# Optimization experiments

Measured on AMD Instinct MI355X. Metric: run time of the kernel, lower is better.

## Reference

```python
import jax, jax.numpy as jnp
import numpy as np

WS = 8
NUM_HEADS = 8
EMBED_DIM = 256
LN_EPS = 1e-5


def setup_inputs() -> dict:
    key = jax.random.key(0)
    ks = jax.random.split(key, 5)
    b, c, h, w = 4, EMBED_DIM, 128, 128
    return {
        "x": jax.random.normal(ks[0], (b, c, h, w), dtype=jnp.float32),
        "in_proj_w": jax.random.normal(ks[1], (3 * c, c), dtype=jnp.float32) * 0.02,
        "in_proj_b": jax.random.normal(ks[2], (3 * c,), dtype=jnp.float32) * 0.02,
        "out_w": jax.random.normal(ks[3], (c, c), dtype=jnp.float32) * 0.02,
        "out_b": jax.random.normal(ks[4], (c,), dtype=jnp.float32) * 0.02,
        "ln_w": jnp.ones((c,), dtype=jnp.float32),
        "ln_b": jnp.zeros((c,), dtype=jnp.float32),
    }


def reference(x, in_proj_w, in_proj_b, out_w, out_b, ln_w, ln_b):
    b, c, h, w = x.shape
    pad_h = (-h) % WS
    pad_w = (-w) % WS
    xp = jnp.pad(x, ((0, 0), (0, 0), (0, pad_h), (0, pad_w)))
    Hp, Wp = h + pad_h, w + pad_w
    h1, w1 = Hp // WS, Wp // WS
    L = h1 * w1            # attention sequence = number of windows
    N = b * WS * WS        # attention batch = b * within-window positions
    # rearrange 'b c (h1 h2) (w1 w2) -> (h1 w1) (b h2 w2) c', then batch-first
    t = xp.reshape(b, c, h1, WS, w1, WS)
    t = jnp.transpose(t, (2, 4, 0, 3, 5, 1)).reshape(L, N, c)
    t = jnp.transpose(t, (1, 0, 2))  # [N, L, c]
    # nn.MultiheadAttention (self-attention, no mask)
    qkv = t @ in_proj_w.T + in_proj_b  # [N, L, 3c]
    q, k, v = jnp.split(qkv, 3, axis=-1)
    D = c // NUM_HEADS
    q = q.reshape(N, L, NUM_HEADS, D) * (D ** -0.5)
    k = k.reshape(N, L, NUM_HEADS, D)
    v = v.reshape(N, L, NUM_HEADS, D)
    attn = jax.nn.softmax(jnp.einsum('nlhd,nmhd->nhlm', q, k), axis=-1)
    o = jnp.einsum('nhlm,nmhd->nlhd', attn, v).reshape(N, L, c)
    o = o @ out_w.T + out_b
    # LayerNorm over channel dim
    mu = jnp.mean(o, axis=-1, keepdims=True)
    var = jnp.mean(jnp.square(o - mu), axis=-1, keepdims=True)
    o = (o - mu) * jax.lax.rsqrt(var + LN_EPS) * ln_w + ln_b
    # inverse rearrange '(h1 w1) (b h2 w2) c -> b c (h1 h2) (w1 w2)'
    y = jnp.transpose(o, (1, 0, 2)).reshape(h1, w1, b, WS, WS, c)
    y = jnp.transpose(y, (2, 5, 0, 3, 1, 4)).reshape(b, c, Hp, Wp)
    return y[:, :, :h, :w]
```

## Files before the change

### kernel.cpp

```cpp
#include <hip/hip_runtime.h>
#include <stdint.h>
#include <stddef.h>


typedef __attribute__((ext_vector_type(8))) short bf16x8;
typedef __attribute__((ext_vector_type(4))) float f32x4;
typedef __attribute__((ext_vector_type(16))) float f32x16;
typedef __attribute__((ext_vector_type(4))) unsigned u32x4;
typedef __attribute__((ext_vector_type(2))) unsigned u32x2;
typedef unsigned short bf16u;

#define LOG2E 1.4426950408889634f
#define MFMA32(a, b, c) __builtin_amdgcn_mfma_f32_32x32x16_bf16(a, b, c, 0, 0, 0)

__device__ __forceinline__ bf16u f2b(float f) {
  uint32_t u = __float_as_uint(f);
  u += 0x7fffu + ((u >> 16) & 1u);
  return (bf16u)(u >> 16);
}
__device__ __forceinline__ float b2f(bf16u s) {
  return __uint_as_float(((uint32_t)s) << 16);
}

__device__ __forceinline__ void gload_lds16(const void* g, void* l) {
  __builtin_amdgcn_global_load_lds((__attribute__((address_space(1))) void*)(g),
                                   (__attribute__((address_space(3))) void*)(l),
                                   16, 0, 0);
}

__device__ __forceinline__ unsigned cvtpk(float a, float b) {
  unsigned r;
  asm("v_cvt_pk_bf16_f32 %0, %1, %2" : "=v"(r) : "v"(a), "v"(b));
  return r;
}

__device__ __forceinline__ float frcp(float x) {
  float r;
  asm("v_rcp_f32 %0, %1" : "=v"(r) : "v"(x));
  return r;
}

__device__ __forceinline__ void swap32(unsigned a, unsigned b, bool hi,
                                       unsigned& x, unsigned& y) {
#if __has_builtin(__builtin_amdgcn_permlane32_swap)
  typedef __attribute__((ext_vector_type(2))) unsigned uint2v;
  uint2v r = __builtin_amdgcn_permlane32_swap(a, b, false, false);
  x = r.x;
  y = r.y;
#else
  unsigned as = (unsigned)__shfl_xor((int)a, 32);
  unsigned bs = (unsigned)__shfl_xor((int)b, 32);
  x = hi ? bs : a;
  y = hi ? b : as;
#endif
}

__global__ __launch_bounds__(256) void k_convert2(const float* __restrict__ s1,
                                                  const float* __restrict__ s2,
                                                  bf16u* __restrict__ d1,
                                                  bf16u* __restrict__ d2) {
  int i = blockIdx.x * 256 + threadIdx.x;
  if (i < 768 * 256) d1[i] = f2b(s1[i]);
  else { int j = i - 768 * 256; d2[j] = f2b(s2[j]); }
}

__global__ __launch_bounds__(256) void k_rearrange(const float* __restrict__ x,
                                                   bf16u* __restrict__ Tb) {
  const int bid = blockIdx.x;
  const int ct = bid & 7, hh = (bid >> 3) & 127, b = bid >> 10;
  const int c0 = ct * 32;
  const int h1 = hh >> 3, h2 = hh & 7;
  __shared__ float tile[32][129];
  for (int e = threadIdx.x; e < 4096; e += 256) {
    int cc = e >> 7, ww = e & 127;
    tile[cc][ww] = x[(((size_t)(b * 256 + c0 + cc)) * 128 + hh) * 128 + ww];
  }
  __syncthreads();
  for (int e = threadIdx.x; e < 4096; e += 256) {
    int ww = e >> 5, cc = e & 31;
    int w1 = ww >> 3, w2 = ww & 7;
    int i = ((b * 64 + h2 * 8 + w2) << 8) | (h1 * 16 + w1);
    Tb[(size_t)i * 256 + c0 + cc] = f2b(tile[cc][ww]);
  }
}

__global__ __launch_bounds__(256) void k_qkv(const bf16u* __restrict__ Tb,
                                             const bf16u* __restrict__ Wb,
                                             const float* __restrict__ bias,
                                             bf16u* __restrict__ Qb,
                                             bf16u* __restrict__ Kb,
                                             bf16u* __restrict__ Vtb) {
  __shared__ bf16u As[128 * 64];
  __shared__ bf16u Bs[128 * 64];
  const int bid0 = blockIdx.x;
  const int bid = (bid0 & 7) * 384 + (bid0 >> 3);
  const int o0 = (bid % 6) * 128;
  const int i0 = (bid / 6) * 128;
  const int seg = o0 >> 8;
  const int t = threadIdx.x;
  const int lane = t & 63, lo = lane & 15, hi = lane >> 4;
  const int w = t >> 6, wr = w >> 1, wc = w & 1;
  const int rr = t >> 3, cc8 = t & 7;
  f32x4 acc[4][4] = {};
  for (int k0 = 0; k0 < 256; k0 += 64) {
    __syncthreads();
#pragma unroll
    for (int j = 0; j < 4; ++j) {
      const int row = j * 32 + rr;
      const int sc = (cc8 ^ (row & 7)) * 8;
      bf16u* const da = As + (j * 32 + w * 8) * 64;
      bf16u* const db = Bs + (j * 32 + w * 8) * 64;
      gload_lds16(Tb + (size_t)(i0 + row) * 256 + k0 + sc, da);
      gload_lds16(Wb + (size_t)(o0 + row) * 256 + k0 + sc, db);
    }
    __syncthreads();
#pragma unroll
    for (int ks = 0; ks < 2; ++ks) {
      bf16x8 af[4], bf_[4];
#pragma unroll
      for (int m = 0; m < 4; ++m) {
        const int row = wr * 64 + m * 16 + lo;
        const int c = (ks * 4 + hi) ^ (lo & 7);
        af[m] = *(const bf16x8*)&As[row * 64 + c * 8];
      }
#pragma unroll
      for (int nn = 0; nn < 4; ++nn) {
        const int row = wc * 64 + nn * 16 + lo;
        const int c = (ks * 4 + hi) ^ (lo & 7);
        bf_[nn] = *(const bf16x8*)&Bs[row * 64 + c * 8];
      }
#pragma unroll
      for (int m = 0; m < 4; ++m)
#pragma unroll
        for (int nn = 0; nn < 4; ++nn)
          acc[m][nn] = __builtin_amdgcn_mfma_f32_16x16x32_bf16(af[m], bf_[nn], acc[m][nn], 0, 0, 0);
    }
  }
  const float oscale = (seg == 0) ? (0.17677669529663687f * LOG2E) : 1.0f;
#pragma unroll
  for (int m = 0; m < 4; ++m) {
#pragma unroll
    for (int nn = 0; nn < 4; ++nn) {
      const int o = o0 + wc * 64 + nn * 16 + lo;
      const int within = o & 255, head = within >> 5, dd = within & 31;
      const float bia = bias[o];
      const int tok0 = i0 + wr * 64 + m * 16 + hi * 4;
      const int nt = tok0 >> 8, ls0 = tok0 & 255;
      if (seg == 2) {
        float v0 = acc[m][nn][0] + bia, v1 = acc[m][nn][1] + bia;
        float v2 = acc[m][nn][2] + bia, v3 = acc[m][nn][3] + bia;
        u32x2 pkd = {cvtpk(v0, v1), cvtpk(v2, v3)};
        *(u32x2*)(Vtb + ((size_t)((nt * 8 + head) * 32 + dd)) * 256 + ls0) = pkd;
      } else {
        bf16u* const dst = (seg == 0) ? Qb : Kb;
#pragma unroll
        for (int r = 0; r < 4; ++r) {
          float v = (acc[m][nn][r] + bia) * oscale;
          dst[((size_t)((nt * 8 + head) * 256 + ls0 + r)) * 32 + dd] = f2b(v);
        }
      }
    }
  }
}

__global__ __launch_bounds__(256, 2) void k_attn(const bf16u* __restrict__ Qb,
                                                 const bf16u* __restrict__ Kb,
                                                 const bf16u* __restrict__ Vtb,
                                                 bf16u* __restrict__ Ob) {
  const int nh = blockIdx.x;
  const int n = nh >> 3, h = nh & 7;
  const bf16u* Qp = Qb + (size_t)nh * 8192;
  const bf16u* Kp = Kb + (size_t)nh * 8192;
  const bf16u* Vp = Vtb + (size_t)nh * 8192;
  const int t = threadIdx.x, w = t >> 6, lane = t & 63;
  const int l31 = lane & 31;
  const bool hi5 = (lane & 32) != 0;

  bf16x8 qf[2][2];
#pragma unroll
  for (int qs = 0; qs < 2; ++qs)
#pragma unroll
    for (int dh = 0; dh < 2; ++dh)
      qf[qs][dh] = *(const bf16x8*)(Qp + (size_t)(w * 64 + qs * 32 + l31) * 32 +
                                    dh * 16 + (hi5 ? 8 : 0));

  const bf16u* kbase = Kp + (size_t)l31 * 32 + (hi5 ? 8 : 0);
  const bf16u* vbase = Vp + (size_t)l31 * 256 + (hi5 ? 8 : 0);

  bf16x8 kf0 = *(const bf16x8*)(kbase);
  bf16x8 kf1 = *(const bf16x8*)(kbase + 16);
  bf16x8 vf0 = *(const bf16x8*)(vbase);
  bf16x8 vf1 = *(const bf16x8*)(vbase + 16);

  const u32x4 onesu = {0x3f803f80u, 0x3f803f80u, 0x3f803f80u, 0x3f803f80u};
  const bf16x8 onesf = __builtin_bit_cast(bf16x8, onesu);

  f32x16 accO[2] = {};
  f32x16 accS[2] = {};

#pragma unroll
  for (int kt = 0; kt < 8; ++kt) {
    const int nkt = (kt + 1) & 7;
    bf16x8 nk0 = *(const bf16x8*)(kbase + nkt * 1024);
    bf16x8 nk1 = *(const bf16x8*)(kbase + nkt * 1024 + 16);
    bf16x8 nv0 = *(const bf16x8*)(vbase + nkt * 32);
    bf16x8 nv1 = *(const bf16x8*)(vbase + nkt * 32 + 16);

#pragma unroll
    for (int qs = 0; qs < 2; ++qs) {
      f32x16 s = {};
      s = MFMA32(kf0, qf[qs][0], s);
      s = MFMA32(kf1, qf[qs][1], s);
      unsigned pk[8];
#pragma unroll
      for (int jp = 0; jp < 8; ++jp)
        pk[jp] = cvtpk(exp2f(s[2 * jp]), exp2f(s[2 * jp + 1]));
      unsigned x0, x1, x2, x3, y0, y1, y2, y3;
      swap32(pk[0], pk[2], hi5, x0, x2);
      swap32(pk[1], pk[3], hi5, x1, x3);
      swap32(pk[4], pk[6], hi5, y0, y2);
      swap32(pk[5], pk[7], hi5, y1, y3);
      u32x4 pa0 = {x0, x1, x2, x3};
      u32x4 pa1 = {y0, y1, y2, y3};
      const bf16x8 a0 = __builtin_bit_cast(bf16x8, pa0);
      const bf16x8 a1 = __builtin_bit_cast(bf16x8, pa1);
      __builtin_amdgcn_s_setprio(1);
      accO[qs] = MFMA32(a0, vf0, accO[qs]);
      accO[qs] = MFMA32(a1, vf1, accO[qs]);
      accS[qs] = MFMA32(a0, onesf, accS[qs]);
      accS[qs] = MFMA32(a1, onesf, accS[qs]);
      __builtin_amdgcn_s_setprio(0);
    }
    kf0 = nk0;
    kf1 = nk1;
    vf0 = nv0;
    vf1 = nv1;
  }
#pragma unroll
  for (int qs = 0; qs < 2; ++qs) {
#pragma unroll
    for (int r = 0; r < 16; ++r) {
      int row = (r & 3) + 8 * (r >> 2) + ((lane & 32) >> 3);
      float o = accO[qs][r] * frcp(accS[qs][r]);
      Ob[((size_t)(n * 256 + w * 64 + qs * 32 + row)) * 256 + h * 32 + l31] = f2b(o);
    }
  }
}

__global__ __launch_bounds__(256) void k_out(const bf16u* __restrict__ Ob,
                                             const bf16u* __restrict__ Wb,
                                             const float* __restrict__ bias,
                                             const float* __restrict__ lnw,
                                             const float* __restrict__ lnb,
                                             bf16u* __restrict__ On) {
  __shared__ bf16u As[64 * 64];
  __shared__ bf16u Bs[256 * 64];
  __shared__ float red[64][4][2];
  const int i0 = blockIdx.x * 64;
  const int t = threadIdx.x, w = t >> 6, lane = t & 63, lo = lane & 15, hi = lane >> 4;
  const int rr = t >> 3, cc8 = t & 7;
  f32x4 acc[4][4] = {};
  for (int k0 = 0; k0 < 256; k0 += 64) {
    __syncthreads();
#pragma unroll
    for (int j = 0; j < 2; ++j) {
      const int row = j * 32 + rr;
      const int sc = (cc8 ^ (row & 7)) * 8;
      gload_lds16(Ob + (size_t)(i0 + row) * 256 + k0 + sc,
                  As + (j * 32 + w * 8) * 64);
    }
#pragma unroll
    for (int j = 0; j < 8; ++j) {
      const int row = j * 32 + rr;
      const int sc = (cc8 ^ (row & 7)) * 8;
      gload_lds16(Wb + (size_t)row * 256 + k0 + sc,
                  Bs + (j * 32 + w * 8) * 64);
    }
    __syncthreads();
#pragma unroll
    for (int ks = 0; ks < 2; ++ks) {
      bf16x8 af[4], bf_[4];
#pragma unroll
      for (int m = 0; m < 4; ++m) {
        const int row = m * 16 + lo;
        const int c = (ks * 4 + hi) ^ (lo & 7);
        af[m] = *(const bf16x8*)&As[row * 64 + c * 8];
      }
#pragma unroll
      for (int nn = 0; nn < 4; ++nn) {
        const int row = w * 64 + nn * 16 + lo;
        const int c = (ks * 4 + hi) ^ (lo & 7);
        bf_[nn] = *(const bf16x8*)&Bs[row * 64 + c * 8];
      }
#pragma unroll
      for (int m = 0; m < 4; ++m)
#pragma unroll
        for (int nn = 0; nn < 4; ++nn)
          acc[m][nn] = __builtin_amdgcn_mfma_f32_16x16x32_bf16(af[m], bf_[nn], acc[m][nn], 0, 0, 0);
    }
  }
#pragma unroll
  for (int m = 0; m < 4; ++m)
#pragma unroll
    for (int nn = 0; nn < 4; ++nn) {
      float bia = bias[w * 64 + nn * 16 + lo];
#pragma unroll
      for (int r = 0; r < 4; ++r) acc[m][nn][r] += bia;
    }
#pragma unroll
  for (int m = 0; m < 4; ++m)
#pragma unroll
    for (int r = 0; r < 4; ++r) {
      float sv = acc[m][0][r] + acc[m][1][r] + acc[m][2][r] + acc[m][3][r];
      float sq = acc[m][0][r] * acc[m][0][r] + acc[m][1][r] * acc[m][1][r] +
                 acc[m][2][r] * acc[m][2][r] + acc[m][3][r] * acc[m][3][r];
      sv += __shfl_xor(sv, 1); sq += __shfl_xor(sq, 1);
      sv += __shfl_xor(sv, 2); sq += __shfl_xor(sq, 2);
      sv += __shfl_xor(sv, 4); sq += __shfl_xor(sq, 4);
      sv += __shfl_xor(sv, 8); sq += __shfl_xor(sq, 8);
      if (lo == 0) {
        red[m * 16 + hi * 4 + r][w][0] = sv;
        red[m * 16 + hi * 4 + r][w][1] = sq;
      }
    }
  __syncthreads();
#pragma unroll
  for (int m = 0; m < 4; ++m)
#pragma unroll
    for (int r = 0; r < 4; ++r) {
      int row = m * 16 + hi * 4 + r;
      float S  = red[row][0][0] + red[row][1][0] + red[row][2][0] + red[row][3][0];
      float Q2 = red[row][0][1] + red[row][1][1] + red[row][2][1] + red[row][3][1];
      float mu = S * 0.00390625f;
      float var = Q2 * 0.00390625f - mu * mu;
      float rstd = rsqrtf(var + 1e-5f);
#pragma unroll
      for (int nn = 0; nn < 4; ++nn) {
        int oc = w * 64 + nn * 16 + lo;
        float o = (acc[m][nn][r] - mu) * rstd * lnw[oc] + lnb[oc];
        On[(size_t)(i0 + row) * 256 + oc] = f2b(o);
      }
    }
}

__global__ __launch_bounds__(256) void k_unrearrange(const bf16u* __restrict__ On,
                                                     float* __restrict__ y) {
  const int bid = blockIdx.x;
  const int ct = bid & 7, hh = (bid >> 3) & 127, b = bid >> 10;
  const int c0 = ct * 32;
  const int h1 = hh >> 3, h2 = hh & 7;
  __shared__ float tile[32][129];
  for (int e = threadIdx.x; e < 4096; e += 256) {
    int ww = e >> 5, cc = e & 31;
    int w1 = ww >> 3, w2 = ww & 7;
    int i = ((b * 64 + h2 * 8 + w2) << 8) | (h1 * 16 + w1);
    tile[cc][ww] = b2f(On[(size_t)i * 256 + c0 + cc]);
  }
  __syncthreads();
  for (int e = threadIdx.x; e < 4096; e += 256) {
    int cc = e >> 7, ww = e & 127;
    y[(((size_t)(b * 256 + c0 + cc)) * 128 + hh) * 128 + ww] = tile[cc][ww];
  }
}

extern "C" void kernel_launch(void* const* d_in, const int* in_sizes, int n_in,
                              void* d_out, int out_size, void* d_ws, size_t ws_size,
                              hipStream_t stream) {
  const float* x     = (const float*)d_in[0];
  const float* w_qkv = (const float*)d_in[1];
  const float* b_qkv = (const float*)d_in[2];
  const float* w_out = (const float*)d_in[3];
  const float* b_out = (const float*)d_in[4];
  const float* ln_w  = (const float*)d_in[5];
  const float* ln_b  = (const float*)d_in[6];
  float* y = (float*)d_out;

  const size_t SEG = 33554432;
  char* ws = (char*)d_ws;
  if (ws_size < 5 * SEG + 768 * 256 * 2 + 256 * 256 * 2) return;
  bf16u* Tb = (bf16u*)(ws);
  bf16u* Qb = (bf16u*)(ws + SEG);
  bf16u* Kb = (bf16u*)(ws + 2 * SEG);
  bf16u* Vtb = (bf16u*)(ws + 3 * SEG);
  bf16u* Ob = (bf16u*)(ws + 4 * SEG);
  bf16u* Wqkvb = (bf16u*)(ws + 5 * SEG);
  bf16u* Woutb = (bf16u*)(ws + 5 * SEG + 768 * 256 * 2);
  bf16u* On = Tb;

  k_convert2<<<1024, 256, 0, stream>>>(w_qkv, w_out, Wqkvb, Woutb);
  k_rearrange<<<4096, 256, 0, stream>>>(x, Tb);
  k_qkv<<<3072, 256, 0, stream>>>(Tb, Wqkvb, b_qkv, Qb, Kb, Vtb);
  k_attn<<<2048, 256, 0, stream>>>(Qb, Kb, Vtb, Ob);
  k_out<<<1024, 256, 0, stream>>>(Ob, Woutb, b_out, ln_w, ln_b, On);
  k_unrearrange<<<4096, 256, 0, stream>>>(On, y);
}
```

Baseline: 176.2 us.

## Double-buffer QKV GEMM LDS tiles and raise MFMA wave priority

```diff
diff --git a/kernel.cpp b/kernel.cpp
--- a/kernel.cpp
+++ b/kernel.cpp
@@ -90,8 +90,8 @@
                                              bf16u* __restrict__ Qb,
                                              bf16u* __restrict__ Kb,
                                              bf16u* __restrict__ Vtb) {
-  __shared__ bf16u As[128 * 64];
-  __shared__ bf16u Bs[128 * 64];
+  __shared__ bf16u As[2][128 * 64];
+  __shared__ bf16u Bs[2][128 * 64];
   const int bid0 = blockIdx.x;
   const int bid = (bid0 & 7) * 384 + (bid0 >> 3);
   const int o0 = (bid % 6) * 128;
@@ -101,19 +101,29 @@
   const int lane = t & 63, lo = lane & 15, hi = lane >> 4;
   const int w = t >> 6, wr = w >> 1, wc = w & 1;
   const int rr = t >> 3, cc8 = t & 7;
+  const int sdst = (t & 192) * 8;
+
   f32x4 acc[4][4] = {};
-  for (int k0 = 0; k0 < 256; k0 += 64) {
-    __syncthreads();
-#pragma unroll
-    for (int j = 0; j < 4; ++j) {
-      const int row = j * 32 + rr;
-      const int sc = (cc8 ^ (row & 7)) * 8;
-      bf16u* const da = As + (j * 32 + w * 8) * 64;
-      bf16u* const db = Bs + (j * 32 + w * 8) * 64;
-      gload_lds16(Tb + (size_t)(i0 + row) * 256 + k0 + sc, da);
-      gload_lds16(Wb + (size_t)(o0 + row) * 256 + k0 + sc, db);
-    }
-    __syncthreads();
+
+#define QKV_STAGE(buf, k0)                                                   \
+  {                                                                          \
+    _Pragma("unroll")                                                        \
+    for (int j = 0; j < 4; ++j) {                                            \
+      const int row = j * 32 + rr;                                           \
+      const int sc = (cc8 ^ (row & 7)) * 8;                                  \
+      gload_lds16(Tb + (size_t)(i0 + row) * 256 + (k0) + sc,                 \
+                  As[buf] + j * 2048 + sdst);                                \
+      gload_lds16(Wb + (size_t)(o0 + row) * 256 + (k0) + sc,                 \
+                  Bs[buf] + j * 2048 + sdst);                                \
+    }                                                                        \
+  }
+
+  QKV_STAGE(0, 0);
+  __syncthreads();
+  int cur = 0;
+#pragma unroll
+  for (int it = 0; it < 4; ++it) {
+    if (it < 3) QKV_STAGE(cur ^ 1, (it + 1) * 64);
 #pragma unroll
     for (int ks = 0; ks < 2; ++ks) {
       bf16x8 af[4], bf_[4];
@@ -121,21 +131,27 @@
       for (int m = 0; m < 4; ++m) {
         const int row = wr * 64 + m * 16 + lo;
         const int c = (ks * 4 + hi) ^ (lo & 7);
-        af[m] = *(const bf16x8*)&As[row * 64 + c * 8];
+        af[m] = *(const bf16x8*)&As[cur][row * 64 + c * 8];
       }
 #pragma unroll
       for (int nn = 0; nn < 4; ++nn) {
         const int row = wc * 64 + nn * 16 + lo;
         const int c = (ks * 4 + hi) ^ (lo & 7);
-        bf_[nn] = *(const bf16x8*)&Bs[row * 64 + c * 8];
-      }
+        bf_[nn] = *(const bf16x8*)&Bs[cur][row * 64 + c * 8];
+      }
+      __builtin_amdgcn_s_setprio(1);
 #pragma unroll
       for (int m = 0; m < 4; ++m)
 #pragma unroll
         for (int nn = 0; nn < 4; ++nn)
           acc[m][nn] = __builtin_amdgcn_mfma_f32_16x16x32_bf16(af[m], bf_[nn], acc[m][nn], 0, 0, 0);
-    }
-  }
+      __builtin_amdgcn_s_setprio(0);
+    }
+    __syncthreads();
+    cur ^= 1;
+  }
+#undef QKV_STAGE
+
   const float oscale = (seg == 0) ? (0.17677669529663687f * LOG2E) : 1.0f;
 #pragma unroll
   for (int m = 0; m < 4; ++m) {
```

After: 174.4 us. About the same (-1.0%).
